# Kernel optimization log

Hardware: AMD Instinct MI355X
Metric: run time of the kernel (lower is better)

## Reference

```python
import jax, jax.numpy as jnp
import numpy as np

DIM = 1024
NUM_HEADS = 16
HEAD_DIM = DIM // NUM_HEADS
SCALE = HEAD_DIM ** -0.5


def setup_inputs() -> dict:
    key = jax.random.key(0)
    k1, k2, k3 = jax.random.split(key, 3)
    B, S = 2, 2048
    x = jax.random.normal(k1, (B, S, DIM), dtype=jnp.float32)
    # nn.Linear(dim, 3*dim, bias=False): store as [in, out] for x @ W
    w_qkv = jax.random.normal(k2, (DIM, 3 * DIM), dtype=jnp.float32) * (DIM ** -0.5)
    w_out = jax.random.normal(k3, (DIM, DIM), dtype=jnp.float32) * (DIM ** -0.5)
    return {"x": x, "w_qkv": w_qkv, "w_out": w_out}


def reference(x, w_qkv, w_out):
    B, S, _ = x.shape
    qkv = x @ w_qkv                               # [B,S,3*D]
    q, k, v = jnp.split(qkv, 3, axis=-1)          # each [B,S,D]
    def heads(t):
        return t.reshape(B, S, NUM_HEADS, HEAD_DIM).transpose(0, 2, 1, 3)  # [B,H,S,d]
    q, k, v = heads(q), heads(k), heads(v)
    scores = jnp.einsum('bhqd,bhkd->bhqk', q, k) * SCALE   # [B,H,S,S]
    probs = jax.nn.softmax(scores, axis=-1)
    out = jnp.einsum('bhqk,bhkd->bhqd', probs, v)          # [B,H,S,d]
    out = out.transpose(0, 2, 1, 3).reshape(B, S, DIM)
    return out @ w_out
```

## Files before the change

### kernel.cpp

```cpp
#include <hip/hip_runtime.h>


typedef __bf16 bf16x8 __attribute__((ext_vector_type(8)));
typedef __bf16 bf16x4 __attribute__((ext_vector_type(4)));
typedef float floatx4 __attribute__((ext_vector_type(4)));

#define MFMA16(a, b, c) __builtin_amdgcn_mfma_f32_16x16x32_bf16((a), (b), (c), 0, 0, 0)

#if defined(__has_builtin)
#if __has_builtin(__builtin_amdgcn_exp2f)
#define EXP2F __builtin_amdgcn_exp2f
#endif
#endif
#ifndef EXP2F
#define EXP2F exp2f
#endif

__device__ __forceinline__ unsigned pk_bf16(float a, float b) {
  union { float f; unsigned u; } ua, ub;
  ua.f = a; ub.f = b;
#if defined(__has_builtin) && __has_builtin(__builtin_amdgcn_perm)
  return __builtin_amdgcn_perm(ub.u + 0x8000u, ua.u + 0x8000u, 0x07060302u);
#else
  return ((ua.u + 0x8000u) >> 16) | ((ub.u + 0x8000u) & 0xFFFF0000u);
#endif
}

__device__ __forceinline__ void gl_lds16(const void* g, void* l) {
  __builtin_amdgcn_global_load_lds((__attribute__((address_space(1))) void*)(g),
                                   (__attribute__((address_space(3))) void*)(l),
                                   16, 0, 0);
}

__global__ __launch_bounds__(256) void prep(const float* __restrict__ x,
                                            const float* __restrict__ w_qkv,
                                            const float* __restrict__ w_out,
                                            __bf16* __restrict__ xb,
                                            __bf16* __restrict__ wqkvt,
                                            __bf16* __restrict__ woutt) {
  __shared__ float tile[64][65];
  const int bid = blockIdx.x, t = threadIdx.x;
  if (bid < 4096) {
    int i = (bid * 256 + t) * 4;
    float4 v = *(const float4*)(x + i);
    bf16x4 o = { (__bf16)v.x, (__bf16)v.y, (__bf16)v.z, (__bf16)v.w };
    *(bf16x4*)(xb + i) = o;
    return;
  }
  const float* w;
  __bf16* wt;
  int K = 1024, N, k0, n0;
  if (bid < 4864) {
    int i = bid - 4096;
    w = w_qkv; wt = wqkvt; N = 3072; k0 = (i & 15) * 64; n0 = (i >> 4) * 64;
  } else {
    int i = bid - 4864;
    w = w_out; wt = woutt; N = 1024; k0 = (i & 15) * 64; n0 = (i >> 4) * 64;
  }
  for (int j = 0; j < 16; ++j) {
    int e = j * 256 + t, r = e >> 6, c = e & 63;
    tile[r][c] = w[(size_t)(k0 + r) * N + n0 + c];
  }
  __syncthreads();
  for (int j = 0; j < 16; ++j) {
    int e = j * 256 + t, r = e >> 6, c = e & 63;
    wt[(size_t)(n0 + r) * K + k0 + c] = (__bf16)tile[c][r];
  }
}

__global__ __launch_bounds__(256) void gemm_qkv(const __bf16* __restrict__ A,
                                                const __bf16* __restrict__ Bt,
                                                __bf16* __restrict__ qkb,
                                                __bf16* __restrict__ vt) {
  constexpr int K = 1024;
  constexpr float QSCALE = 0.18033688f;
  __shared__ __align__(16) __bf16 aS[128 * 32];
  __shared__ __align__(16) __bf16 bS[128 * 32];
  const int t = threadIdx.x;
  const int lane = t & 63, wave = t >> 6;
  const int l15 = lane & 15, quad = lane >> 4;
  const int wm = wave >> 1, wn = wave & 1;
  const int m0 = blockIdx.y * 128, n0 = blockIdx.x * 128;

  const floatx4 fzero = {0.f, 0.f, 0.f, 0.f};
  floatx4 acc[4][4];
  for (int mt = 0; mt < 4; ++mt)
    for (int nt = 0; nt < 4; ++nt) acc[mt][nt] = fzero;

  const int arow = t >> 2;
  const int ach = ((t & 3) ^ (arow & 3)) * 8;
  const __bf16* gA0 = A + (size_t)(m0 + arow) * K + ach;
  const __bf16* gA1 = gA0 + (size_t)64 * K;
  const __bf16* gB0 = Bt + (size_t)(n0 + arow) * K + ach;
  const __bf16* gB1 = gB0 + (size_t)64 * K;
  const int swz = (quad ^ (l15 & 3)) * 8;

  for (int k0 = 0; k0 < K; k0 += 32) {
    __syncthreads();
    gl_lds16(gA0 + k0, (char*)aS + t * 16);
    gl_lds16(gA1 + k0, (char*)aS + 4096 + t * 16);
    gl_lds16(gB0 + k0, (char*)bS + t * 16);
    gl_lds16(gB1 + k0, (char*)bS + 4096 + t * 16);
    __syncthreads();

    bf16x8 af[4], bfr[4];
    for (int mt = 0; mt < 4; ++mt)
      af[mt] = *(const bf16x8*)(aS + (wm * 64 + mt * 16 + l15) * 32 + swz);
    for (int nt = 0; nt < 4; ++nt)
      bfr[nt] = *(const bf16x8*)(bS + (wn * 64 + nt * 16 + l15) * 32 + swz);
    for (int mt = 0; mt < 4; ++mt)
      for (int nt = 0; nt < 4; ++nt)
        acc[mt][nt] = MFMA16(af[mt], bfr[nt], acc[mt][nt]);
  }

  for (int mt = 0; mt < 4; ++mt) {
    int row = m0 + wm * 64 + mt * 16 + quad * 4;
    for (int nt = 0; nt < 4; ++nt) {
      int col0 = n0 + wn * 64 + nt * 16;
      if (col0 >= 2048) {
        int dfull = col0 + l15 - 2048;
        int bh = ((row >> 11) << 4) + (dfull >> 6);
        int d = dfull & 63, s0 = row & 2047;
        bf16x4 pk = { (__bf16)acc[mt][nt][0], (__bf16)acc[mt][nt][1],
                      (__bf16)acc[mt][nt][2], (__bf16)acc[mt][nt][3] };
        *(bf16x4*)(vt + ((size_t)bh * 64 + d) * 2048 + s0) = pk;
      } else {
        float sc = (col0 < 1024) ? QSCALE : 1.0f;
        int col = col0 + l15;
        __bf16* cp = qkb + (size_t)row * 2048 + col;
        for (int r = 0; r < 4; ++r) cp[(size_t)r * 2048] = (__bf16)(acc[mt][nt][r] * sc);
      }
    }
  }
}

__global__ __launch_bounds__(256) void gemm_n64(const __bf16* __restrict__ A,
                                                const __bf16* __restrict__ Bt,
                                                float* __restrict__ C) {
  constexpr int K = 1024, N = 1024;
  __shared__ __align__(16) __bf16 aS[128 * 32];
  __shared__ __align__(16) __bf16 bS[64 * 32];
  const int t = threadIdx.x;
  const int lane = t & 63, wave = t >> 6;
  const int l15 = lane & 15, quad = lane >> 4;
  const int m0 = blockIdx.y * 128, n0 = blockIdx.x * 64;

  const floatx4 fzero = {0.f, 0.f, 0.f, 0.f};
  floatx4 acc[2][4];
  for (int mt = 0; mt < 2; ++mt)
    for (int nt = 0; nt < 4; ++nt) acc[mt][nt] = fzero;

  const int arow = t >> 2;
  const int ach = ((t & 3) ^ (arow & 3)) * 8;
  const __bf16* gA0 = A + (size_t)(m0 + arow) * K + ach;
  const __bf16* gA1 = gA0 + (size_t)64 * K;
  const __bf16* gB0 = Bt + (size_t)(n0 + arow) * K + ach;
  const int swz = (quad ^ (l15 & 3)) * 8;

  for (int k0 = 0; k0 < K; k0 += 32) {
    __syncthreads();
    gl_lds16(gA0 + k0, (char*)aS + t * 16);
    gl_lds16(gA1 + k0, (char*)aS + 4096 + t * 16);
    gl_lds16(gB0 + k0, (char*)bS + t * 16);
    __syncthreads();

    bf16x8 af[2], bfr[4];
    for (int mt = 0; mt < 2; ++mt)
      af[mt] = *(const bf16x8*)(aS + (wave * 32 + mt * 16 + l15) * 32 + swz);
    for (int nt = 0; nt < 4; ++nt)
      bfr[nt] = *(const bf16x8*)(bS + (nt * 16 + l15) * 32 + swz);
    for (int mt = 0; mt < 2; ++mt)
      for (int nt = 0; nt < 4; ++nt)
        acc[mt][nt] = MFMA16(af[mt], bfr[nt], acc[mt][nt]);
  }

  for (int mt = 0; mt < 2; ++mt) {
    int row = m0 + wave * 32 + mt * 16 + quad * 4;
    for (int nt = 0; nt < 4; ++nt) {
      int col = n0 + nt * 16 + l15;
      float* cp = C + (size_t)row * N + col;
      for (int r = 0; r < 4; ++r) cp[(size_t)r * N] = acc[mt][nt][r];
    }
  }
}

__global__ __launch_bounds__(256) void flash_attn(const __bf16* __restrict__ qkb,
                                                  const __bf16* __restrict__ vt,
                                                  __bf16* __restrict__ out) {
  __shared__ __align__(16) __bf16 kS[2 * 64 * 64];
  __shared__ __align__(16) __bf16 vS[2 * 64 * 64];
  __shared__ __align__(16) __bf16 pT[4 * 16 * 64];

  const int t = threadIdx.x;
  const int lane = t & 63, wave = t >> 6;
  const int l15 = lane & 15, quad = lane >> 4;
  const int id = blockIdx.x;
  const int xcd = id & 7, slot = id >> 3;
  const int bh = xcd * 4 + (slot >> 4), qb = slot & 15;
  const int b = bh >> 4, h = bh & 15;

  bf16x8 qf[2][2];
  for (int qt = 0; qt < 2; ++qt) {
    const __bf16* qp = qkb +
        (size_t)(b * 2048 + qb * 128 + wave * 32 + qt * 16 + l15) * 2048 + h * 64 + quad * 8;
    qf[qt][0] = *(const bf16x8*)qp;
    qf[qt][1] = *(const bf16x8*)(qp + 32);
  }

  bf16x8 onef;
  for (int j = 0; j < 8; ++j) onef[j] = (__bf16)1.0f;

  const floatx4 fzero = {0.f, 0.f, 0.f, 0.f};
  floatx4 oacc[2][4], lacc[2];
  for (int qt = 0; qt < 2; ++qt) {
    lacc[qt] = fzero;
    for (int dt = 0; dt < 4; ++dt) oacc[qt][dt] = fzero;
  }

  const int srow = t >> 3, schk = (t & 7) ^ (srow & 7);
  const __bf16* kg0 =
      qkb + (size_t)(b * 2048 + srow) * 2048 + 1024 + h * 64 + schk * 8;
  const __bf16* kg1 = kg0 + (size_t)32 * 2048;
  const __bf16* vg0 =
      vt + (size_t)bh * 64 * 2048 + (size_t)srow * 2048 + schk * 8;
  const __bf16* vg1 = vg0 + (size_t)32 * 2048;

  const int l7 = l15 & 7;
  __bf16* pw = pT + wave * 1024 + l15 * 64;

  gl_lds16(kg0, (char*)kS + t * 16);
  gl_lds16(kg1, (char*)kS + 4096 + t * 16);
  gl_lds16(vg0, (char*)vS + t * 16);
  gl_lds16(vg1, (char*)vS + 4096 + t * 16);

  for (int nb = 0; nb < 32; ++nb) {
    __syncthreads();

    if (nb < 31) {
      const size_t n1 = (size_t)(nb + 1) * 64;
      const int oB = ((nb + 1) & 1) * 8192;
      gl_lds16(kg0 + n1 * 2048, (char*)kS + oB + t * 16);
      gl_lds16(kg1 + n1 * 2048, (char*)kS + oB + 4096 + t * 16);
      gl_lds16(vg0 + n1, (char*)vS + oB + t * 16);
      gl_lds16(vg1 + n1, (char*)vS + oB + 4096 + t * 16);
    }

    const __bf16* kC = kS + (nb & 1) * 4096;
    const __bf16* vC = vS + (nb & 1) * 4096;

    bf16x8 kf[4][2];
    for (int nt = 0; nt < 4; ++nt)
      for (int ks = 0; ks < 2; ++ks)
        kf[nt][ks] = *(const bf16x8*)(kC + (nt * 16 + l15) * 64 +
                                      ((ks * 4 + quad) ^ l7) * 8);
    bf16x8 vf[2][4];
    for (int ks = 0; ks < 2; ++ks)
      for (int dt = 0; dt < 4; ++dt)
        vf[ks][dt] = *(const bf16x8*)(vC + (dt * 16 + l15) * 64 +
                                      ((ks * 4 + quad) ^ l7) * 8);

    for (int qt = 0; qt < 2; ++qt) {
      floatx4 sa[4];
      for (int nt = 0; nt < 4; ++nt) {
        floatx4 a = fzero;
        a = MFMA16(kf[nt][0], qf[qt][0], a);
        a = MFMA16(kf[nt][1], qf[qt][1], a);
        sa[nt] = a;
      }
      for (int nt = 0; nt < 4; ++nt) {
        float p0 = EXP2F(sa[nt][0]);
        float p1 = EXP2F(sa[nt][1]);
        float p2 = EXP2F(sa[nt][2]);
        float p3 = EXP2F(sa[nt][3]);
        unsigned w0 = pk_bf16(p0, p1);
        unsigned w1 = pk_bf16(p2, p3);
        uint2 wv = {w0, w1};
        *(uint2*)((char*)pw + (((nt * 2 + (quad >> 1)) ^ l7) * 16 + (quad & 1) * 8)) = wv;
      }
      for (int ks = 0; ks < 2; ++ks) {
        bf16x8 pa = *(const bf16x8*)(pw + ((ks * 4 + quad) ^ l7) * 8);
        for (int dt = 0; dt < 4; ++dt)
          oacc[qt][dt] = MFMA16(pa, vf[ks][dt], oacc[qt][dt]);
        lacc[qt] = MFMA16(pa, onef, lacc[qt]);
      }
    }
  }

  for (int qt = 0; qt < 2; ++qt) {
    float inv[4];
    for (int r = 0; r < 4; ++r) inv[r] = 1.f / lacc[qt][r];
    __bf16* ob = out +
        (size_t)(b * 2048 + qb * 128 + wave * 32 + qt * 16 + quad * 4) * 1024 + h * 64;
    for (int dt = 0; dt < 4; ++dt)
      for (int r = 0; r < 4; ++r)
        ob[(size_t)r * 1024 + dt * 16 + l15] = (__bf16)(oacc[qt][dt][r] * inv[r]);
  }
}

extern "C" void kernel_launch(void* const* d_in, const int* in_sizes, int n_in,
                              void* d_out, int out_size, void* d_ws, size_t ws_size,
                              hipStream_t stream) {
  const float* x = (const float*)d_in[0];
  const float* w_qkv = (const float*)d_in[1];
  const float* w_out = (const float*)d_in[2];
  float* out = (float*)d_out;

  char* ws = (char*)d_ws;
  __bf16* xb = (__bf16*)(ws);
  __bf16* wqkvt = (__bf16*)(ws + ((size_t)8 << 20));
  __bf16* qkb = (__bf16*)(ws + ((size_t)16 << 20));
  __bf16* vtg = (__bf16*)(ws + ((size_t)32 << 20));
  __bf16* aout = (__bf16*)(ws + ((size_t)40 << 20));
  __bf16* woutt = (__bf16*)(ws + ((size_t)48 << 20));

  prep<<<5120, 256, 0, stream>>>(x, w_qkv, w_out, xb, wqkvt, woutt);
  gemm_qkv<<<dim3(24, 32), 256, 0, stream>>>(xb, wqkvt, qkb, vtg);
  flash_attn<<<512, 256, 0, stream>>>(qkb, vtg, aout);
  gemm_n64<<<dim3(16, 32), 256, 0, stream>>>(aout, woutt, out);
}
```

Before: 190.6 us.

## Split attention KV range into two groups and merge with combine kernel

The flash attention kernel now processes only half of the key/value sequence per block, doubling the grid to 1024 blocks for better CU occupancy on the GPU. Each half writes unnormalized fp16 partial outputs and fp32 row sums into workspace. A new combine kernel adds the two halves and normalizes into the bf16 attention output. This adds an extra launch and roughly 24MB of extra memory traffic, and relies on the softmax having no running max so partial sums can simply be added.

```diff
diff --git a/kernel.cpp b/kernel.cpp
--- a/kernel.cpp
+++ b/kernel.cpp
@@ -4,6 +4,7 @@
 typedef __bf16 bf16x8 __attribute__((ext_vector_type(8)));
 typedef __bf16 bf16x4 __attribute__((ext_vector_type(4)));
 typedef float floatx4 __attribute__((ext_vector_type(4)));
+typedef _Float16 f16x8 __attribute__((ext_vector_type(8)));
 
 #define MFMA16(a, b, c) __builtin_amdgcn_mfma_f32_16x16x32_bf16((a), (b), (c), 0, 0, 0)
 
@@ -186,7 +187,8 @@
 
 __global__ __launch_bounds__(256) void flash_attn(const __bf16* __restrict__ qkb,
                                                   const __bf16* __restrict__ vt,
-                                                  __bf16* __restrict__ out) {
+                                                  _Float16* __restrict__ oPart,
+                                                  float* __restrict__ lPart) {
   __shared__ __align__(16) __bf16 kS[2 * 64 * 64];
   __shared__ __align__(16) __bf16 vS[2 * 64 * 64];
   __shared__ __align__(16) __bf16 pT[4 * 16 * 64];
@@ -196,7 +198,8 @@
   const int l15 = lane & 15, quad = lane >> 4;
   const int id = blockIdx.x;
   const int xcd = id & 7, slot = id >> 3;
-  const int bh = xcd * 4 + (slot >> 4), qb = slot & 15;
+  const int bhg = xcd * 8 + (slot >> 4), qb = slot & 15;
+  const int bh = bhg >> 1, grp = bhg & 1;
   const int b = bh >> 4, h = bh & 15;
 
   bf16x8 qf[2][2];
@@ -219,10 +222,10 @@
 
   const int srow = t >> 3, schk = (t & 7) ^ (srow & 7);
   const __bf16* kg0 =
-      qkb + (size_t)(b * 2048 + srow) * 2048 + 1024 + h * 64 + schk * 8;
+      qkb + (size_t)(b * 2048 + grp * 1024 + srow) * 2048 + 1024 + h * 64 + schk * 8;
   const __bf16* kg1 = kg0 + (size_t)32 * 2048;
   const __bf16* vg0 =
-      vt + (size_t)bh * 64 * 2048 + (size_t)srow * 2048 + schk * 8;
+      vt + (size_t)bh * 64 * 2048 + (size_t)srow * 2048 + grp * 1024 + schk * 8;
   const __bf16* vg1 = vg0 + (size_t)32 * 2048;
 
   const int l7 = l15 & 7;
@@ -233,10 +236,10 @@
   gl_lds16(vg0, (char*)vS + t * 16);
   gl_lds16(vg1, (char*)vS + 4096 + t * 16);
 
-  for (int nb = 0; nb < 32; ++nb) {
-    __syncthreads();
-
-    if (nb < 31) {
+  for (int nb = 0; nb < 16; ++nb) {
+    __syncthreads();
+
+    if (nb < 15) {
       const size_t n1 = (size_t)(nb + 1) * 64;
       const int oB = ((nb + 1) & 1) * 8192;
       gl_lds16(kg0 + n1 * 2048, (char*)kS + oB + t * 16);
@@ -286,15 +289,33 @@
     }
   }
 
+  _Float16* oP = oPart + (size_t)grp * 4096 * 1024;
+  float* lP = lPart + (size_t)grp * 4096 * 16;
   for (int qt = 0; qt < 2; ++qt) {
-    float inv[4];
-    for (int r = 0; r < 4; ++r) inv[r] = 1.f / lacc[qt][r];
-    __bf16* ob = out +
-        (size_t)(b * 2048 + qb * 128 + wave * 32 + qt * 16 + quad * 4) * 1024 + h * 64;
+    int rowb = qb * 128 + wave * 32 + qt * 16;
+    if (l15 == 0)
+      for (int r = 0; r < 4; ++r)
+        lP[(size_t)(b * 2048 + rowb + quad * 4 + r) * 16 + h] = lacc[qt][r];
+    _Float16* ob = oP + (size_t)(b * 2048 + rowb + quad * 4) * 1024 + h * 64;
     for (int dt = 0; dt < 4; ++dt)
       for (int r = 0; r < 4; ++r)
-        ob[(size_t)r * 1024 + dt * 16 + l15] = (__bf16)(oacc[qt][dt][r] * inv[r]);
-  }
+        ob[(size_t)r * 1024 + dt * 16 + l15] = (_Float16)oacc[qt][dt][r];
+  }
+}
+
+__global__ __launch_bounds__(256) void combine(const _Float16* __restrict__ oPart,
+                                               const float* __restrict__ lPart,
+                                               __bf16* __restrict__ aout) {
+  size_t i = ((size_t)blockIdx.x * 256 + threadIdx.x) * 8;
+  int row = i >> 10, h = (i >> 6) & 15;
+  float l0 = lPart[(size_t)row * 16 + h];
+  float l1 = lPart[(size_t)4096 * 16 + (size_t)row * 16 + h];
+  float inv = 1.f / (l0 + l1);
+  f16x8 a = *(const f16x8*)(oPart + i);
+  f16x8 c = *(const f16x8*)(oPart + (size_t)4096 * 1024 + i);
+  bf16x8 o;
+  for (int j = 0; j < 8; ++j) o[j] = (__bf16)(((float)a[j] + (float)c[j]) * inv);
+  *(bf16x8*)(aout + i) = o;
 }
 
 extern "C" void kernel_launch(void* const* d_in, const int* in_sizes, int n_in,
@@ -308,13 +329,16 @@
   char* ws = (char*)d_ws;
   __bf16* xb = (__bf16*)(ws);
   __bf16* wqkvt = (__bf16*)(ws + ((size_t)8 << 20));
+  _Float16* oPart = (_Float16*)(ws);
   __bf16* qkb = (__bf16*)(ws + ((size_t)16 << 20));
   __bf16* vtg = (__bf16*)(ws + ((size_t)32 << 20));
   __bf16* aout = (__bf16*)(ws + ((size_t)40 << 20));
   __bf16* woutt = (__bf16*)(ws + ((size_t)48 << 20));
+  float* lPart = (float*)(ws + ((size_t)50 << 20));
 
   prep<<<5120, 256, 0, stream>>>(x, w_qkv, w_out, xb, wqkvt, woutt);
   gemm_qkv<<<dim3(24, 32), 256, 0, stream>>>(xb, wqkvt, qkb, vtg);
-  flash_attn<<<512, 256, 0, stream>>>(qkb, vtg, aout);
+  flash_attn<<<1024, 256, 0, stream>>>(qkb, vtg, oPart, lPart);
+  combine<<<2048, 256, 0, stream>>>(oPart, lPart, aout);
   gemm_n64<<<dim3(16, 32), 256, 0, stream>>>(aout, woutt, out);
 }
```

New measurement: 197.0 us. 3.3% more time.
